# Optimization experiments

Measured on AMD Instinct MI355X. Metric: run time of the kernel, lower is better.

## Reference

```python
import jax, jax.numpy as jnp
import numpy as np

EMBED_DIM = 1024
NUM_HEADS = 16
HEAD_DIM = EMBED_DIM // NUM_HEADS
SEQ_LEN = 2048
B = 2


def setup_inputs() -> dict:
    key = jax.random.key(0)
    ks = jax.random.split(key, 6)
    x = jax.random.normal(ks[0], (B, SEQ_LEN, EMBED_DIM), dtype=jnp.float32)
    # Linear params (torch Linear: y = x @ W.T + b); store W as [in, out] for einsum
    qkv_w = jax.random.normal(ks[1], (EMBED_DIM, 3 * EMBED_DIM), dtype=jnp.float32) * (EMBED_DIM ** -0.5)
    qkv_b = jnp.zeros((3 * EMBED_DIM,), dtype=jnp.float32)
    proj_w = jax.random.normal(ks[2], (EMBED_DIM, EMBED_DIM), dtype=jnp.float32) * (EMBED_DIM ** -0.5)
    proj_b = jnp.zeros((EMBED_DIM,), dtype=jnp.float32)
    # relative position bias table [2L-1, H], trunc_normal std=0.02 ~ normal*0.02
    bias_table = jax.random.normal(ks[3], (2 * SEQ_LEN - 1, NUM_HEADS), dtype=jnp.float32) * 0.02
    return {"x": x, "qkv_w": qkv_w, "qkv_b": qkv_b, "proj_w": proj_w, "proj_b": proj_b, "bias_table": bias_table}


def _rel_pos_index(L):
    coords = jnp.arange(L)
    return (coords[None, :] - coords[:, None]) + (SEQ_LEN - 1)  # [L, L] int


def reference(x, qkv_w, qkv_b, proj_w, proj_b, bias_table):
    Bsz, L, C = x.shape
    scale = HEAD_DIM ** -0.5
    qkv = x @ qkv_w + qkv_b                               # [B, L, 3C]
    qkv = qkv.reshape(Bsz, L, 3, NUM_HEADS, HEAD_DIM)
    q = jnp.transpose(qkv[:, :, 0], (0, 2, 1, 3))          # [B, H, L, D]
    k = jnp.transpose(qkv[:, :, 1], (0, 2, 1, 3))
    v = jnp.transpose(qkv[:, :, 2], (0, 2, 1, 3))
    attn = jnp.einsum('bhqd,bhkd->bhqk', q, k) * scale     # [B, H, L, L]
    rel_bias = bias_table[_rel_pos_index(L)]               # [L, L, H]
    attn = attn + jnp.transpose(rel_bias, (2, 0, 1))[None]  # broadcast over batch
    attn = jax.nn.softmax(attn, axis=-1)
    out = jnp.einsum('bhqk,bhkd->bhqd', attn, v)           # [B, H, L, D]
    out = jnp.transpose(out, (0, 2, 1, 3)).reshape(Bsz, L, C)
    return out @ proj_w + proj_b
```

## Files before the change

### kernel.cpp

```cpp
#include <hip/hip_runtime.h>
#include <type_traits>

typedef short bf16x4 __attribute__((ext_vector_type(4)));
typedef short bf16x8 __attribute__((ext_vector_type(8)));
typedef float f32x4 __attribute__((ext_vector_type(4)));
typedef float f32x8 __attribute__((ext_vector_type(8)));
typedef float f32x16 __attribute__((ext_vector_type(16)));

__device__ __forceinline__ unsigned short f2bf(float f) {
  union { float f; unsigned int u; } v; v.f = f;
  unsigned int r = v.u + 0x7FFFu + ((v.u >> 16) & 1u);
  return (unsigned short)(r >> 16);
}

__device__ __forceinline__ float exp2_fast(float x) {
  float r;
  asm("v_exp_f32 %0, %1" : "=v"(r) : "v"(x));
  return r;
}

__device__ __forceinline__ unsigned int cvt_pk_bf16(float lo, float hi) {
  unsigned int r;
  asm("v_cvt_pk_bf16_f32 %0, %1, %2" : "=v"(r) : "v"(lo), "v"(hi));
  return r;
}


__global__ __launch_bounds__(256) void k_transpose_bf16(const float* __restrict__ in,
                                                        unsigned short* __restrict__ out,
                                                        int R, int C) {
  __shared__ float tile[32][33];
  int tx = threadIdx.x, ty = threadIdx.y;
  int c0 = blockIdx.x * 32, r0 = blockIdx.y * 32;
#pragma unroll
  for (int i = 0; i < 32; i += 8) tile[ty + i][tx] = in[(size_t)(r0 + ty + i) * C + c0 + tx];
  __syncthreads();
#pragma unroll
  for (int i = 0; i < 32; i += 8) out[(size_t)(c0 + ty + i) * R + r0 + tx] = f2bf(tile[tx][ty + i]);
}

__global__ __launch_bounds__(256) void k_bias_cols(const float* __restrict__ bt,
                                                   float* __restrict__ bh) {
  int i = blockIdx.x * 256 + threadIdx.x;
  if (i < 4095 * 16) bh[(i & 15) * 4096 + (i >> 4)] = bt[i] * 1.44269504089f;
}

template <int EPI>
__global__ __launch_bounds__(512) void k_gemm(const void* __restrict__ Ain,
                                              const unsigned short* __restrict__ Bt,
                                              const float* __restrict__ bias,
                                              float* __restrict__ Cf,
                                              unsigned short* __restrict__ qb,
                                              unsigned short* __restrict__ kb,
                                              unsigned short* __restrict__ vtb) {
  __shared__ unsigned short Alds[2][128 * 64];
  __shared__ unsigned short Blds[2][128 * 64];
  const int t = threadIdx.x;
  const int l = t & 63, w = t >> 6;
  const int l15 = l & 15, l4 = l >> 4;
  const int wm = w >> 2, wn = w & 3;

  const int hwid = blockIdx.x;
  const int x = hwid & 7, loc = hwid >> 3;
  const int bm = ((x >> 1) * 8 + (loc & 7)) * 128;
  const int bn = ((x & 1) * (EPI ? 12 : 4) + (loc >> 3)) * 128;

  const int srow = t >> 3;
  const int sc = t & 7;
  using AELT = typename std::conditional<EPI == 1, float, unsigned short>::type;
  using AREG = typename std::conditional<EPI == 1, f32x8, bf16x8>::type;
  const AELT* aglp = ((const AELT*)Ain) + (size_t)(bm + srow) * 1024 + sc * 8;
  const unsigned short* bgl = Bt + (size_t)(bn + srow) * 1024 + sc * 8;
  const int wls = srow * 64 + ((sc ^ (srow & 7)) * 8);

  f32x4 acc[4][2];
#pragma unroll
  for (int i = 0; i < 4; ++i)
#pragma unroll
    for (int j = 0; j < 2; ++j) acc[i][j] = (f32x4){0.f, 0.f, 0.f, 0.f};

  AREG ra_a[2], rb_a[2];
  bf16x8 ra_b[2], rb_b[2];

#define GLOAD(RA, RB, KT)                                                     \
  _Pragma("unroll") for (int q = 0; q < 2; ++q) {                             \
    RA[q] = *(const AREG*)(aglp + (size_t)q * 65536 + (KT) * 64);             \
    RB[q] = *(const bf16x8*)(bgl + (size_t)q * 65536 + (KT) * 64);            \
  }
#define SWRITE(RA, RB, CUR)                                                   \
  _Pragma("unroll") for (int q = 0; q < 2; ++q) {                             \
    bf16x8 aw;                                                                \
    if constexpr (EPI == 1) {                                                 \
      union { unsigned int u[4]; bf16x8 v; } pk;                              \
      pk.u[0] = cvt_pk_bf16(RA[q][0], RA[q][1]);                              \
      pk.u[1] = cvt_pk_bf16(RA[q][2], RA[q][3]);                              \
      pk.u[2] = cvt_pk_bf16(RA[q][4], RA[q][5]);                              \
      pk.u[3] = cvt_pk_bf16(RA[q][6], RA[q][7]);                              \
      aw = pk.v;                                                              \
    } else {                                                                  \
      aw = RA[q];                                                             \
    }                                                                         \
    *(bf16x8*)&Alds[CUR][q * 4096 + wls] = aw;                                \
    *(bf16x8*)&Blds[CUR][q * 4096 + wls] = RB[q];                             \
  }

  GLOAD(ra_a, ra_b, 0);
  GLOAD(rb_a, rb_b, 1);
  SWRITE(ra_a, ra_b, 0);
  asm volatile("s_waitcnt lgkmcnt(0)" ::: "memory");
  __builtin_amdgcn_s_barrier();

#define GEMM_PHASE(KT, RFA, RFB, RPA, RPB)                                    \
  {                                                                           \
    const int cur_ = (KT) & 1;                                                \
    if ((KT) + 2 < 16) { GLOAD(RFA, RFB, (KT) + 2); }                         \
    __builtin_amdgcn_s_setprio(1);                                            \
    _Pragma("unroll") for (int kc = 0; kc < 2; ++kc) {                        \
      bf16x8 af[4], bv[2];                                                    \
      _Pragma("unroll") for (int i = 0; i < 4; ++i) {                         \
        int ra_ = wm * 64 + i * 16 + l15;                                     \
        af[i] = *(const bf16x8*)&Alds[cur_][ra_ * 64 +                        \
                                            (((kc * 4 + l4) ^ (l15 & 7))) * 8]; \
      }                                                                       \
      _Pragma("unroll") for (int j = 0; j < 2; ++j) {                         \
        int rb_ = wn * 32 + j * 16 + l15;                                     \
        bv[j] = *(const bf16x8*)&Blds[cur_][rb_ * 64 +                        \
                                            (((kc * 4 + l4) ^ (l15 & 7))) * 8]; \
      }                                                                       \
      _Pragma("unroll") for (int i = 0; i < 4; ++i)                           \
        _Pragma("unroll") for (int jn = 0; jn < 2; ++jn)                      \
          acc[i][jn] =                                                        \
              __builtin_amdgcn_mfma_f32_16x16x32_bf16(af[i], bv[jn],          \
                                                      acc[i][jn], 0, 0, 0);   \
    }                                                                         \
    __builtin_amdgcn_s_setprio(0);                                            \
    if ((KT) + 1 < 16) { SWRITE(RPA, RPB, cur_ ^ 1); }                        \
    asm volatile("s_waitcnt lgkmcnt(0)" ::: "memory");                        \
    __builtin_amdgcn_s_barrier();                                             \
  }

  for (int kt = 0; kt < 16; kt += 2) {
    GEMM_PHASE(kt, ra_a, ra_b, rb_a, rb_b);
    GEMM_PHASE(kt + 1, rb_a, rb_b, ra_a, ra_b);
  }
#undef GEMM_PHASE
#undef SWRITE
#undef GLOAD

#pragma unroll
  for (int i = 0; i < 4; ++i) {
#pragma unroll
    for (int jn = 0; jn < 2; ++jn) {
      int n = bn + wn * 32 + jn * 16 + l15;
      float bval = bias[n];
#pragma unroll
      for (int j = 0; j < 4; ++j) {
        int m = bm + wm * 64 + i * 16 + l4 * 4 + j;
        float v = acc[i][jn][j] + bval;
        if (EPI == 0) {
          Cf[(size_t)m * 1024 + n] = v;
        } else {
          int which = n >> 10, hh = (n >> 6) & 15, d = n & 63;
          int bb = m >> 11, pos = m & 2047;
          int bhh = bb * 16 + hh;
          if (which == 0)
            qb[((size_t)bhh * 2048 + pos) * 64 + d] = f2bf(v * 0.18033688f);
          else if (which == 1)
            kb[((size_t)bhh * 2048 + pos) * 64 + d] = f2bf(v);
          else
            vtb[((size_t)bhh * 64 + d) * 2048 + pos] = f2bf(v);
        }
      }
    }
  }
}

__global__ __launch_bounds__(256) void k_attn(const unsigned short* __restrict__ qbuf,
                                              const unsigned short* __restrict__ kbuf,
                                              const unsigned short* __restrict__ vtbuf,
                                              const float* __restrict__ biash,
                                              unsigned short* __restrict__ aout) {
  __shared__ __align__(16) unsigned short Klds[2][64 * 64];
  __shared__ __align__(16) unsigned short Vlds[2][64 * 64];

  const int t = threadIdx.x;
  const int w = t >> 6, l = t & 63;
  const int l31 = l & 31, hi = l >> 5;

  const int bid = blockIdx.x;
  const int swzb = (bid & 7) * 64 + (bid >> 3);
  const int qt = swzb & 15;
  const int bh = swzb >> 4;
  const int h = bh & 15, b = bh >> 4;
  const int qbase = qt * 128;
  const int wq = qbase + w * 32;

  bf16x8 qB[4];
  {
    const unsigned short* qrow = qbuf + ((size_t)bh * 2048 + wq + l31) * 64;
#pragma unroll
    for (int ds = 0; ds < 4; ++ds) qB[ds] = *(const bf16x8*)&qrow[ds * 16 + hi * 8];
  }

  f32x16 O[2];
#pragma unroll
  for (int i = 0; i < 16; ++i) { O[0][i] = 0.f; O[1][i] = 0.f; }
  float m_run = -3e38f, l_run = 0.f;

  const int c0r = t >> 3, c0c = t & 7;
  const unsigned short* kg = kbuf + ((size_t)bh * 2048 + c0r) * 64 + c0c * 8;
  const unsigned short* vg = vtbuf + ((size_t)bh * 64 + c0r) * 2048 + c0c * 8;
  const int wKV = c0r * 64 + ((c0c ^ (c0r & 7)) * 8);

  {
    bf16x8 k0 = *(const bf16x8*)(kg);
    bf16x8 k1 = *(const bf16x8*)(kg + 32 * 64);
    bf16x8 v0 = *(const bf16x8*)(vg);
    bf16x8 v1 = *(const bf16x8*)(vg + 32 * 2048);
    *(bf16x8*)&Klds[0][wKV] = k0;
    *(bf16x8*)&Klds[0][wKV + 2048] = k1;
    *(bf16x8*)&Vlds[0][wKV] = v0;
    *(bf16x8*)&Vlds[0][wKV + 2048] = v1;
  }
  __syncthreads();

  const float* bgl = biash + h * 4096 + 2047 - (wq + l31) + 4 * hi;

  for (int kt = 0; kt < 32; ++kt) {
    const int cur = kt & 1;

    bf16x8 kst0, kst1, vst0, vst1;
    if (kt < 31) {
      const unsigned short* kga = kg + (size_t)(kt + 1) * 4096;
      const unsigned short* vga = vg + (kt + 1) * 64;
      kst0 = *(const bf16x8*)(kga);
      kst1 = *(const bf16x8*)(kga + 32 * 64);
      vst0 = *(const bf16x8*)(vga);
      vst1 = *(const bf16x8*)(vga + 32 * 2048);
    }
    const int kbase = kt * 64;

    f32x4 bq[2][4];
#pragma unroll
    for (int kt2 = 0; kt2 < 2; ++kt2)
#pragma unroll
      for (int g = 0; g < 4; ++g)
        __builtin_memcpy(&bq[kt2][g], &bgl[kbase + 32 * kt2 + 8 * g], 16);

    f32x16 sacc[2];
#pragma unroll
    for (int i = 0; i < 16; ++i) { sacc[0][i] = 0.f; sacc[1][i] = 0.f; }
    __builtin_amdgcn_s_setprio(1);
#pragma unroll
    for (int kt2 = 0; kt2 < 2; ++kt2) {
      int row = kt2 * 32 + l31;
      int rsw = row & 7;
#pragma unroll
      for (int ds = 0; ds < 4; ++ds) {
        bf16x8 ka = *(const bf16x8*)&Klds[cur][row * 64 + (((2 * ds + hi) ^ rsw) * 8)];
        sacc[kt2] = __builtin_amdgcn_mfma_f32_32x32x16_bf16(ka, qB[ds], sacc[kt2], 0, 0, 0);
      }
    }
    __builtin_amdgcn_s_setprio(0);

#pragma unroll
    for (int kt2 = 0; kt2 < 2; ++kt2)
#pragma unroll
      for (int g = 0; g < 4; ++g)
#pragma unroll
        for (int r = 0; r < 4; ++r) sacc[kt2][4 * g + r] += bq[kt2][g][r];

    float mx;
    {
      float q0 = fmaxf(fmaxf(sacc[0][0], sacc[0][1]), fmaxf(sacc[0][2], sacc[0][3]));
      float q1 = fmaxf(fmaxf(sacc[0][4], sacc[0][5]), fmaxf(sacc[0][6], sacc[0][7]));
      float q2 = fmaxf(fmaxf(sacc[0][8], sacc[0][9]), fmaxf(sacc[0][10], sacc[0][11]));
      float q3 = fmaxf(fmaxf(sacc[0][12], sacc[0][13]), fmaxf(sacc[0][14], sacc[0][15]));
      float q4 = fmaxf(fmaxf(sacc[1][0], sacc[1][1]), fmaxf(sacc[1][2], sacc[1][3]));
      float q5 = fmaxf(fmaxf(sacc[1][4], sacc[1][5]), fmaxf(sacc[1][6], sacc[1][7]));
      float q6 = fmaxf(fmaxf(sacc[1][8], sacc[1][9]), fmaxf(sacc[1][10], sacc[1][11]));
      float q7 = fmaxf(fmaxf(sacc[1][12], sacc[1][13]), fmaxf(sacc[1][14], sacc[1][15]));
      mx = fmaxf(fmaxf(fmaxf(q0, q1), fmaxf(q2, q3)), fmaxf(fmaxf(q4, q5), fmaxf(q6, q7)));
      mx = fmaxf(mx, __shfl_xor(mx, 32));
    }

    if (__any(mx > m_run + 8.f)) {
      float mnew = fmaxf(m_run, mx);
      float alpha = exp2_fast(m_run - mnew);
      m_run = mnew;
      l_run *= alpha;
#pragma unroll
      for (int g = 0; g < 4; ++g)
#pragma unroll
        for (int r = 0; r < 4; ++r) {
          float a_lo = __shfl(alpha, 8 * g + r);
          float a_hi = __shfl(alpha, 8 * g + r + 4);
          float aq = hi ? a_hi : a_lo;
          O[0][4 * g + r] *= aq;
          O[1][4 * g + r] *= aq;
        }
    }

#pragma unroll
    for (int kt2 = 0; kt2 < 2; ++kt2)
#pragma unroll
      for (int i = 0; i < 16; ++i) sacc[kt2][i] = exp2_fast(sacc[kt2][i] - m_run);
    {
      float s0 = (sacc[0][0] + sacc[0][1]) + (sacc[0][2] + sacc[0][3]);
      float s1 = (sacc[0][4] + sacc[0][5]) + (sacc[0][6] + sacc[0][7]);
      float s2 = (sacc[0][8] + sacc[0][9]) + (sacc[0][10] + sacc[0][11]);
      float s3 = (sacc[0][12] + sacc[0][13]) + (sacc[0][14] + sacc[0][15]);
      float s4 = (sacc[1][0] + sacc[1][1]) + (sacc[1][2] + sacc[1][3]);
      float s5 = (sacc[1][4] + sacc[1][5]) + (sacc[1][6] + sacc[1][7]);
      float s6 = (sacc[1][8] + sacc[1][9]) + (sacc[1][10] + sacc[1][11]);
      float s7 = (sacc[1][12] + sacc[1][13]) + (sacc[1][14] + sacc[1][15]);
      float rs = ((s0 + s1) + (s2 + s3)) + ((s4 + s5) + (s6 + s7));
      rs += __shfl_xor(rs, 32);
      l_run += rs;
    }

    bf16x8 pa[2][2];
#pragma unroll
    for (int kt2 = 0; kt2 < 2; ++kt2)
#pragma unroll
      for (int mm = 0; mm < 2; ++mm) {
        union { unsigned int u[4]; bf16x8 v; } pk;
        pk.u[0] = cvt_pk_bf16(sacc[kt2][8 * mm + 0], sacc[kt2][8 * mm + 1]);
        pk.u[1] = cvt_pk_bf16(sacc[kt2][8 * mm + 2], sacc[kt2][8 * mm + 3]);
        pk.u[2] = cvt_pk_bf16(sacc[kt2][8 * mm + 4], sacc[kt2][8 * mm + 5]);
        pk.u[3] = cvt_pk_bf16(sacc[kt2][8 * mm + 6], sacc[kt2][8 * mm + 7]);
        pa[kt2][mm] = pk.v;
      }

    __builtin_amdgcn_s_setprio(1);
#pragma unroll
    for (int dt = 0; dt < 2; ++dt) {
      int row = dt * 32 + l31;
      int rsw = row & 7;
#pragma unroll
      for (int kt2 = 0; kt2 < 2; ++kt2)
#pragma unroll
        for (int mm = 0; mm < 2; ++mm) {
          int cA = (4 * kt2 + 2 * mm) ^ rsw;
          int cB = (4 * kt2 + 2 * mm + 1) ^ rsw;
          bf16x4 vlo = *(const bf16x4*)&Vlds[cur][row * 64 + cA * 8 + 4 * hi];
          bf16x4 vhi = *(const bf16x4*)&Vlds[cur][row * 64 + cB * 8 + 4 * hi];
          bf16x8 vb = __builtin_shufflevector(vlo, vhi, 0, 1, 2, 3, 4, 5, 6, 7);
          O[dt] = __builtin_amdgcn_mfma_f32_32x32x16_bf16(pa[kt2][mm], vb, O[dt], 0, 0, 0);
        }
    }
    __builtin_amdgcn_s_setprio(0);

    if (kt < 31) {
      *(bf16x8*)&Klds[cur ^ 1][wKV] = kst0;
      *(bf16x8*)&Klds[cur ^ 1][wKV + 2048] = kst1;
      *(bf16x8*)&Vlds[cur ^ 1][wKV] = vst0;
      *(bf16x8*)&Vlds[cur ^ 1][wKV + 2048] = vst1;
    }
    __syncthreads();
  }

  {
    float linv = 1.f / l_run;
#pragma unroll
    for (int g = 0; g < 4; ++g)
#pragma unroll
      for (int r = 0; r < 4; ++r) {
        float v_lo = __shfl(linv, 8 * g + r);
        float v_hi = __shfl(linv, 8 * g + r + 4);
        float sc = hi ? v_hi : v_lo;
        int q = wq + 8 * g + r + 4 * hi;
        size_t base = ((size_t)b * 2048 + q) * 1024 + h * 64 + l31;
        aout[base] = f2bf(O[0][4 * g + r] * sc);
        aout[base + 32] = f2bf(O[1][4 * g + r] * sc);
      }
  }
}


extern "C" void kernel_launch(void* const* d_in, const int* in_sizes, int n_in,
                              void* d_out, int out_size, void* d_ws, size_t ws_size,
                              hipStream_t stream) {
  const float* x = (const float*)d_in[0];
  const float* qkv_w = (const float*)d_in[1];
  const float* qkv_b = (const float*)d_in[2];
  const float* proj_w = (const float*)d_in[3];
  const float* proj_b = (const float*)d_in[4];
  const float* bias_table = (const float*)d_in[5];
  float* out = (float*)d_out;

  char* ws = (char*)d_ws;
  unsigned short* attn_out = (unsigned short*)(ws);
  unsigned short* wqkv = (unsigned short*)(ws + (size_t)(8u << 20));
  unsigned short* wproj = (unsigned short*)(ws + (size_t)(14u << 20));
  unsigned short* qb = (unsigned short*)(ws + (size_t)(16u << 20));
  unsigned short* kb = (unsigned short*)(ws + (size_t)(24u << 20));
  unsigned short* vtb = (unsigned short*)(ws + (size_t)(32u << 20));
  float* biash = (float*)(ws + (size_t)(40u << 20));

  k_transpose_bf16<<<dim3(96, 32), dim3(32, 8), 0, stream>>>(qkv_w, wqkv, 1024, 3072);
  k_transpose_bf16<<<dim3(32, 32), dim3(32, 8), 0, stream>>>(proj_w, wproj, 1024, 1024);
  k_bias_cols<<<dim3(256), dim3(256), 0, stream>>>(bias_table, biash);

  k_gemm<1><<<dim3(768), dim3(512), 0, stream>>>((const void*)x, wqkv, qkv_b, nullptr, qb, kb,
                                                 vtb);
  k_attn<<<dim3(512), dim3(256), 0, stream>>>(qb, kb, vtb, biash, attn_out);
  k_gemm<0><<<dim3(256), dim3(512), 0, stream>>>((const void*)attn_out, wproj, proj_b, out,
                                                 nullptr, nullptr, nullptr);
}
```

Measured before the change: 141.2 us.

## Split attention KV range into two halves with separate merge kernel

Each attention block now processes half of the key sequence, doubling the grid to increase parallelism and occupancy. Unnormalized fp32 partial outputs plus running max and sum are written to workspace, and a new merge kernel combines the two halves and writes bf16 output. This adds substantial extra global memory traffic and an additional kernel launch. The path is used only when the workspace is large enough.

```diff
diff --git a/kernel.cpp b/kernel.cpp
--- a/kernel.cpp
+++ b/kernel.cpp
@@ -175,11 +175,14 @@
   }
 }
 
+template <int SPLIT>
 __global__ __launch_bounds__(256) void k_attn(const unsigned short* __restrict__ qbuf,
                                               const unsigned short* __restrict__ kbuf,
                                               const unsigned short* __restrict__ vtbuf,
                                               const float* __restrict__ biash,
-                                              unsigned short* __restrict__ aout) {
+                                              unsigned short* __restrict__ aout,
+                                              float* __restrict__ Opart,
+                                              float* __restrict__ mlpart) {
   __shared__ __align__(16) unsigned short Klds[2][64 * 64];
   __shared__ __align__(16) unsigned short Vlds[2][64 * 64];
 
@@ -188,12 +191,22 @@
   const int l31 = l & 31, hi = l >> 5;
 
   const int bid = blockIdx.x;
-  const int swzb = (bid & 7) * 64 + (bid >> 3);
-  const int qt = swzb & 15;
-  const int bh = swzb >> 4;
+  int qt, bh, half;
+  if (SPLIT) {
+    const int loc = bid >> 3;
+    bh = (bid & 7) * 4 + (loc >> 5);
+    qt = loc & 15;
+    half = (loc >> 4) & 1;
+  } else {
+    const int swzb = (bid & 7) * 64 + (bid >> 3);
+    qt = swzb & 15;
+    bh = swzb >> 4;
+    half = 0;
+  }
   const int h = bh & 15, b = bh >> 4;
   const int qbase = qt * 128;
   const int wq = qbase + w * 32;
+  const int NT = SPLIT ? 16 : 32;
 
   bf16x8 qB[4];
   {
@@ -208,8 +221,10 @@
   float m_run = -3e38f, l_run = 0.f;
 
   const int c0r = t >> 3, c0c = t & 7;
-  const unsigned short* kg = kbuf + ((size_t)bh * 2048 + c0r) * 64 + c0c * 8;
-  const unsigned short* vg = vtbuf + ((size_t)bh * 64 + c0r) * 2048 + c0c * 8;
+  const unsigned short* kg =
+      kbuf + ((size_t)bh * 2048 + half * 1024 + c0r) * 64 + c0c * 8;
+  const unsigned short* vg =
+      vtbuf + ((size_t)bh * 64 + c0r) * 2048 + half * 1024 + c0c * 8;
   const int wKV = c0r * 64 + ((c0c ^ (c0r & 7)) * 8);
 
   {
@@ -224,13 +239,13 @@
   }
   __syncthreads();
 
-  const float* bgl = biash + h * 4096 + 2047 - (wq + l31) + 4 * hi;
-
-  for (int kt = 0; kt < 32; ++kt) {
+  const float* bgl = biash + h * 4096 + 2047 - (wq + l31) + 4 * hi + half * 1024;
+
+  for (int kt = 0; kt < NT; ++kt) {
     const int cur = kt & 1;
 
     bf16x8 kst0, kst1, vst0, vst1;
-    if (kt < 31) {
+    if (kt < NT - 1) {
       const unsigned short* kga = kg + (size_t)(kt + 1) * 4096;
       const unsigned short* vga = vg + (kt + 1) * 64;
       kst0 = *(const bf16x8*)(kga);
@@ -351,7 +366,7 @@
     }
     __builtin_amdgcn_s_setprio(0);
 
-    if (kt < 31) {
+    if (kt < NT - 1) {
       *(bf16x8*)&Klds[cur ^ 1][wKV] = kst0;
       *(bf16x8*)&Klds[cur ^ 1][wKV + 2048] = kst1;
       *(bf16x8*)&Vlds[cur ^ 1][wKV] = vst0;
@@ -360,7 +375,22 @@
     __syncthreads();
   }
 
-  {
+  if (SPLIT) {
+    float* obase = Opart + (((size_t)half * 32 + bh) * 2048) * 64;
+#pragma unroll
+    for (int g = 0; g < 4; ++g)
+#pragma unroll
+      for (int r = 0; r < 4; ++r) {
+        int q = wq + 8 * g + r + 4 * hi;
+        obase[(size_t)q * 64 + l31] = O[0][4 * g + r];
+        obase[(size_t)q * 64 + 32 + l31] = O[1][4 * g + r];
+      }
+    if (hi == 0) {
+      size_t mi = (((size_t)half * 32 + bh) * 2048 + wq + l31) * 2;
+      mlpart[mi] = m_run;
+      mlpart[mi + 1] = l_run;
+    }
+  } else {
     float linv = 1.f / l_run;
 #pragma unroll
     for (int g = 0; g < 4; ++g)
@@ -375,6 +405,34 @@
         aout[base + 32] = f2bf(O[1][4 * g + r] * sc);
       }
   }
+}
+
+__global__ __launch_bounds__(256) void k_merge(const float* __restrict__ Opart,
+                                               const float* __restrict__ mlpart,
+                                               unsigned short* __restrict__ aout) {
+  int id = blockIdx.x * 256 + threadIdx.x;
+  int dq = id & 15;
+  int q = (id >> 4) & 2047;
+  int bh = id >> 15;
+  int h = bh & 15, b = bh >> 4;
+
+  size_t mi0 = (((size_t)bh) * 2048 + q) * 2;
+  size_t mi1 = (((size_t)32 + bh) * 2048 + q) * 2;
+  float m0 = mlpart[mi0], l0 = mlpart[mi0 + 1];
+  float m1 = mlpart[mi1], l1 = mlpart[mi1 + 1];
+  float m = fmaxf(m0, m1);
+  float a0 = exp2_fast(m0 - m);
+  float a1 = exp2_fast(m1 - m);
+  float linv = 1.f / (l0 * a0 + l1 * a1);
+
+  f32x4 o0, o1;
+  __builtin_memcpy(&o0, Opart + (((size_t)bh) * 2048 + q) * 64 + dq * 4, 16);
+  __builtin_memcpy(&o1, Opart + (((size_t)32 + bh) * 2048 + q) * 64 + dq * 4, 16);
+
+  size_t base = ((size_t)b * 2048 + q) * 1024 + h * 64 + dq * 4;
+#pragma unroll
+  for (int j = 0; j < 4; ++j)
+    aout[base + j] = f2bf((o0[j] * a0 + o1[j] * a1) * linv);
 }
 
 
@@ -397,6 +455,9 @@
   unsigned short* kb = (unsigned short*)(ws + (size_t)(24u << 20));
   unsigned short* vtb = (unsigned short*)(ws + (size_t)(32u << 20));
   float* biash = (float*)(ws + (size_t)(40u << 20));
+  float* Opart = (float*)(ws + (size_t)(41u << 20));
+  float* mlpart = (float*)(ws + (size_t)(76u << 20));
+  const size_t ws_need = (size_t)(79u << 20);
 
   k_transpose_bf16<<<dim3(96, 32), dim3(32, 8), 0, stream>>>(qkv_w, wqkv, 1024, 3072);
   k_transpose_bf16<<<dim3(32, 32), dim3(32, 8), 0, stream>>>(proj_w, wproj, 1024, 1024);
@@ -404,7 +465,13 @@
 
   k_gemm<1><<<dim3(768), dim3(512), 0, stream>>>((const void*)x, wqkv, qkv_b, nullptr, qb, kb,
                                                  vtb);
-  k_attn<<<dim3(512), dim3(256), 0, stream>>>(qb, kb, vtb, biash, attn_out);
+  if (ws_size >= ws_need) {
+    k_attn<1><<<dim3(1024), dim3(256), 0, stream>>>(qb, kb, vtb, biash, nullptr, Opart, mlpart);
+    k_merge<<<dim3(4096), dim3(256), 0, stream>>>(Opart, mlpart, attn_out);
+  } else {
+    k_attn<0><<<dim3(512), dim3(256), 0, stream>>>(qb, kb, vtb, biash, attn_out, nullptr,
+                                                   nullptr);
+  }
   k_gemm<0><<<dim3(256), dim3(512), 0, stream>>>((const void*)attn_out, wproj, proj_b, out,
                                                  nullptr, nullptr, nullptr);
 }
```

Measured after the change: 181.4 us. +28.5%, slower.
